# Kernel optimization log

Measured on AMD Instinct MI355X. Metric: run time of the kernel, lower is better.

The kernel has to match this reference:

```python
import jax, jax.numpy as jnp
import numpy as np

NUM_HEADS = 16


def setup_inputs() -> dict:
    key = jax.random.key(0)
    ks = jax.random.split(key, 5)
    N, L, E = 4, 1024, 1024
    x = jax.random.normal(ks[0], (N, L, E), dtype=jnp.float32)
    sc = 1.0 / np.sqrt(E)
    wq = jax.random.normal(ks[1], (E, E), dtype=jnp.float32) * sc
    wk = jax.random.normal(ks[2], (E, E), dtype=jnp.float32) * sc
    wv = jax.random.normal(ks[3], (E, E), dtype=jnp.float32) * sc
    wo = jax.random.normal(ks[4], (E, E), dtype=jnp.float32) * sc
    return {"x": x, "wq": wq, "wk": wk, "wv": wv, "wo": wo}


def reference(x, wq, wk, wv, wo):
    N, L, E = x.shape
    H = NUM_HEADS
    d = E // H  # d_k = d_v = d_q
    # Linear layers: y = x @ W^T (torch Linear weight is (out, in))
    q = (x @ wq.T).reshape(N, H, L, d)  # NOTE: raw view, matches torch .view
    k = (x @ wk.T).reshape(N, H, L, d)
    v = (x @ wv.T).reshape(N, H, L, d)
    scores = jnp.einsum("nhld,nhmd->nhlm", q, k) / jnp.sqrt(jnp.float32(d))
    # causal mask (dropout is identity in eval / p=0)
    causal = jnp.tril(jnp.ones((L, L), dtype=bool))
    scores = jnp.where(causal, scores, jnp.float32(-jnp.inf))
    attn = jax.nn.softmax(scores, axis=-1)
    wei = jnp.einsum("nhlm,nhmd->nhld", attn, v).reshape(N, L, H * d)
    return wei @ wo.T
```

## Files before the change

### kernel.cpp

```cpp
#include <hip/hip_runtime.h>
#include <hip/hip_bf16.h>

using bf16 = __hip_bfloat16;
typedef __attribute__((ext_vector_type(8))) short bf16x8;
typedef __attribute__((ext_vector_type(4))) float f32x4;

#define MFMA16(a, b, c) __builtin_amdgcn_mfma_f32_16x16x32_bf16(a, b, c, 0, 0, 0)
#define SWZ(row, byteoff) ((byteoff) ^ (((row) & 7) << 4))

__device__ __forceinline__ unsigned short f2b(float f) {
  union { float f; unsigned int u; } c; c.f = f;
  unsigned int r = c.u + 0x7fffu + ((c.u >> 16) & 1u);
  return (unsigned short)(r >> 16);
}
__device__ __forceinline__ float b2f(short b) {
  union { unsigned int u; float f; } c;
  c.u = ((unsigned int)(unsigned short)b) << 16;
  return c.f;
}
__device__ __forceinline__ bf16x8 scale8(bf16x8 v, float s) {
  bf16x8 r;
#pragma unroll
  for (int j = 0; j < 8; ++j) r[j] = (short)f2b(b2f(v[j]) * s);
  return r;
}
__device__ __forceinline__ unsigned cvtpk(float a, float b) {
  unsigned r;
  asm("v_cvt_pk_bf16_f32 %0, %1, %2" : "=v"(r) : "v"(a), "v"(b));
  return r;
}

__device__ __forceinline__ void gload_lds16(const void* g, void* l) {
  __builtin_amdgcn_global_load_lds(
      (const __attribute__((address_space(1))) void*)g,
      (__attribute__((address_space(3))) void*)l, 16, 0, 0);
}

__device__ __forceinline__ void store_out(float* p, float v) { *p = v; }
__device__ __forceinline__ void store_out(bf16* p, float v) {
  *(unsigned short*)p = f2b(v);
}

__global__ __launch_bounds__(256) void cast_all(
    const float* __restrict__ x, const float* __restrict__ wq,
    const float* __restrict__ wk, const float* __restrict__ wv,
    const float* __restrict__ wo,
    unsigned short* __restrict__ xb, unsigned short* __restrict__ wqb,
    unsigned short* __restrict__ wkb, unsigned short* __restrict__ wvb,
    unsigned short* __restrict__ wob) {
  int i = blockIdx.x * 256 + threadIdx.x;
  const float* src;
  unsigned short* dst;
  int off;
  if (i < 1048576) {
    src = x; dst = xb; off = i;
  } else {
    int j = i - 1048576;
    int seg = j >> 18;
    off = j & 262143;
    src = (seg == 0) ? wq : (seg == 1) ? wk : (seg == 2) ? wv : wo;
    dst = (seg == 0) ? wqb : (seg == 1) ? wkb : (seg == 2) ? wvb : wob;
  }
  float4 v = reinterpret_cast<const float4*>(src)[off];
  ushort4 o;
  o.x = f2b(v.x); o.y = f2b(v.y); o.z = f2b(v.z); o.w = f2b(v.w);
  reinterpret_cast<ushort4*>(dst)[off] = o;
}

template <typename TOUT>
__device__ __forceinline__ void gemm_tile(const bf16* __restrict__ A,
                                          const bf16* __restrict__ Bt,
                                          TOUT* __restrict__ C, int N, int K,
                                          int bm, int bn) {
  __shared__ bf16 Asm[128 * 64];
  __shared__ bf16 Bsm[128 * 64];
  const int tid = threadIdx.x;
  const int lane = tid & 63;
  const int w = tid >> 6;
  const int wr = w >> 1, wc = w & 1;
  const int fr = lane & 15;
  const int fg = lane >> 4;
  f32x4 acc[4][4] = {};

  const int strow = w * 8 + (lane >> 3);
  const int stcb = (lane & 7) * 16;

  for (int kt = 0; kt < K; kt += 64) {
#pragma unroll
    for (int r = 0; r < 4; ++r) {
      const int row = r * 32 + strow;
      gload_lds16(
          (const char*)(A + (size_t)(bm + row) * K + kt) + SWZ(row, stcb),
          (char*)Asm + (r * 32 + w * 8) * 128);
      gload_lds16(
          (const char*)(Bt + (size_t)row * K + kt) + SWZ(row, stcb),
          (char*)Bsm + (r * 32 + w * 8) * 128);
    }
    __syncthreads();
    bf16x8 afr[4][2], bfr[4][2];
#pragma unroll
    for (int m = 0; m < 4; ++m) {
      const int row = wr * 64 + m * 16 + fr;
      const char* rp = (const char*)Asm + row * 128;
#pragma unroll
      for (int s = 0; s < 2; ++s)
        afr[m][s] = *(const bf16x8*)(rp + SWZ(row, s * 64 + fg * 16));
    }
#pragma unroll
    for (int n = 0; n < 4; ++n) {
      const int row = wc * 64 + n * 16 + fr;
      const char* rp = (const char*)Bsm + row * 128;
#pragma unroll
      for (int s = 0; s < 2; ++s)
        bfr[n][s] = *(const bf16x8*)(rp + SWZ(row, s * 64 + fg * 16));
    }
    __builtin_amdgcn_s_setprio(1);
#pragma unroll
    for (int m = 0; m < 4; ++m)
#pragma unroll
      for (int n = 0; n < 4; ++n) {
        acc[m][n] = MFMA16(afr[m][0], bfr[n][0], acc[m][n]);
        acc[m][n] = MFMA16(afr[m][1], bfr[n][1], acc[m][n]);
      }
    __builtin_amdgcn_s_setprio(0);
    __syncthreads();
  }
#pragma unroll
  for (int m = 0; m < 4; ++m) {
    const int row0 = bm + wr * 64 + m * 16 + (lane >> 4) * 4;
#pragma unroll
    for (int n = 0; n < 4; ++n) {
      const int col = bn + wc * 64 + n * 16 + fr;
#pragma unroll
      for (int r = 0; r < 4; ++r)
        store_out(&C[(size_t)(row0 + r) * N + col], acc[m][n][r]);
    }
  }
}

__global__ __launch_bounds__(256) void gemm_qkv(
    const bf16* __restrict__ A, const bf16* __restrict__ B3,
    bf16* __restrict__ Cq, bf16* __restrict__ Ck, bf16* __restrict__ Cv) {
  const int id = blockIdx.y * 32 + blockIdx.x;
  const int sw = (id & 7) * 96 + (id >> 3);
  const int bm = (sw & 31) * 128;
  const int bnG = (sw >> 5) * 128;
  bf16* C = (bnG < 1024) ? Cq : (bnG < 2048) ? Ck : Cv;
  gemm_tile<bf16>(A, B3 + (size_t)bnG * 1024, C, 1024, 1024, bm, bnG & 1023);
}

__global__ __launch_bounds__(256) void gemm_out(const bf16* __restrict__ A,
                                                const bf16* __restrict__ B,
                                                float* __restrict__ C) {
  const int id = blockIdx.y * 32 + blockIdx.x;
  const int sw = (id & 7) * 32 + (id >> 3);
  const int bm = (sw & 31) * 128;
  const int bn = (sw >> 5) * 128;
  gemm_tile<float>(A, B + (size_t)bn * 1024, C, 1024, 1024, bm, bn);
}

__global__ __launch_bounds__(256) void attn_fwd(
    const bf16* __restrict__ Q, const bf16* __restrict__ K,
    const bf16* __restrict__ V, bf16* __restrict__ O) {
  const int nh = blockIdx.y;
  const size_t base = (size_t)nh * 65536;
  const bf16* Qp = Q + base;
  const bf16* Kp = K + base;
  const bf16* Vp = V + base;
  bf16* Op = O + base;
  const int p = blockIdx.x;
  const int qiA = p, qiB = 15 - p;
  const int tid = threadIdx.x;
  const int lane = tid & 63;
  const int w = tid >> 6;
  const int fr = lane & 15;
  const int fg = lane >> 4;

  __shared__ bf16 Ksm[2][64 * 64];
  __shared__ bf16 Vts[2][64 * 64];

  const float QSC = 0.125f * 1.44269504089f;
  const float MS = 12.0f;
  const int rA0 = qiA * 64 + w * 16;
  const int rB0 = qiB * 64 + w * 16;
  bf16x8 qA[2], qB[2];
#pragma unroll
  for (int ks = 0; ks < 2; ++ks) {
    qA[ks] = scale8(
        *(const bf16x8*)&Qp[(size_t)(rA0 + fr) * 64 + ks * 32 + fg * 8], QSC);
    qB[ks] = scale8(
        *(const bf16x8*)&Qp[(size_t)(rB0 + fr) * 64 + ks * 32 + fg * 8], QSC);
  }

  float sA = 0.f, sB = 0.f;
  f32x4 oA[4], oB[4];
#pragma unroll
  for (int d = 0; d < 4; ++d) {
    oA[d] = (f32x4){0.f, 0.f, 0.f, 0.f};
    oB[d] = (f32x4){0.f, 0.f, 0.f, 0.f};
  }

  const int NKV = qiB + 1;
  const int qloc = w * 16 + fr;

  const int bkv = (tid & 15) * 4;
  const int bd = (tid >> 4) * 4;
  union VU { ushort4 v; unsigned short s[4]; };
  VU v4[4], nv4[4];

  const int krow = w * 16 + (lane >> 3);
  const int kcb = (lane & 7) * 16;

#define STAGE_K(kt, bi)                                                       \
  {                                                                           \
    _Pragma("unroll") for (int i = 0; i < 2; ++i) {                           \
      const int row = krow + i * 8;                                           \
      gload_lds16((const char*)Kp + ((size_t)((kt)*64 + row) * 128 +          \
                                     SWZ(row, kcb)),                          \
                  (char*)&Ksm[bi][0] + (w * 16 + i * 8) * 128);               \
    }                                                                         \
  }
#define LOAD_V(kt, r)                                                         \
  {                                                                           \
    _Pragma("unroll") for (int j = 0; j < 4; ++j) (r)[j].v =                  \
        *(const ushort4*)(Vp + (size_t)((kt)*64 + bkv + j) * 64 + bd);        \
  }
#define WRITE_V(bi, r)                                                        \
  {                                                                           \
    _Pragma("unroll") for (int i = 0; i < 4; ++i) {                           \
      VU o4;                                                                  \
      _Pragma("unroll") for (int j = 0; j < 4; ++j) o4.s[j] = (r)[j].s[i];    \
      const int row = bd + i;                                                 \
      *(ushort4*)((char*)&Vts[bi][0] + row * 128 + SWZ(row, bkv * 2)) = o4.v; \
    }                                                                         \
  }

  STAGE_K(0, 0);
  LOAD_V(0, v4);
  WRITE_V(0, v4);
  __syncthreads();

  union PU { bf16x8 v; unsigned u[4]; };
  union VF { bf16x8 v; unsigned long long q[2]; };

  for (int kt = 0; kt < NKV; ++kt) {
    const int b = kt & 1;
    const bool more = (kt + 1 < NKV);
    if (more) {
      STAGE_K(kt + 1, b ^ 1);
      LOAD_V(kt + 1, nv4);
    }
    const bool aAct = (kt <= qiA);

    bf16x8 kf[4][2];
#pragma unroll
    for (int c = 0; c < 4; ++c) {
      const int row = c * 16 + fr;
      const char* rp = (const char*)&Ksm[b][0] + row * 128;
      kf[c][0] = *(const bf16x8*)(rp + SWZ(row, fg * 16));
      kf[c][1] = *(const bf16x8*)(rp + SWZ(row, 64 + fg * 16));
    }
    VF vf[4][2];
#pragma unroll
    for (int d = 0; d < 4; ++d) {
      const int row = d * 16 + fr;
      const char* rp = (const char*)&Vts[b][0] + row * 128;
#pragma unroll
      for (int ks = 0; ks < 2; ++ks) {
        vf[d][ks].q[0] =
            *(const unsigned long long*)(rp + SWZ(row, ks * 64 + fg * 8));
        vf[d][ks].q[1] =
            *(const unsigned long long*)(rp + SWZ(row, ks * 64 + 32 + fg * 8));
      }
    }

    auto strip_sm = [&](const bf16x8 (&qf)[2], float& s, bool diag,
                        PU (&pa)[2]) {
      f32x4 sc[4];
      __builtin_amdgcn_s_setprio(1);
#pragma unroll
      for (int c = 0; c < 4; ++c) {
        f32x4 acc = (f32x4){0.f, 0.f, 0.f, 0.f};
        acc = MFMA16(kf[c][0], qf[0], acc);
        acc = MFMA16(kf[c][1], qf[1], acc);
        sc[c] = acc;
      }
      __builtin_amdgcn_s_setprio(0);
      float pv[4][4];
#pragma unroll
      for (int c = 0; c < 4; ++c)
#pragma unroll
        for (int r = 0; r < 4; ++r) {
          float sv = sc[c][r];
          if (diag) {
            const int kvloc = c * 16 + fg * 4 + r;
            sv = (kvloc <= qloc) ? sv : -INFINITY;
          }
          const float e = __builtin_amdgcn_exp2f(sv - MS);
          pv[c][r] = e;
          s += e;
        }
#pragma unroll
      for (int ks = 0; ks < 2; ++ks) {
        pa[ks].u[0] = cvtpk(pv[ks * 2][0], pv[ks * 2][1]);
        pa[ks].u[1] = cvtpk(pv[ks * 2][2], pv[ks * 2][3]);
        pa[ks].u[2] = cvtpk(pv[ks * 2 + 1][0], pv[ks * 2 + 1][1]);
        pa[ks].u[3] = cvtpk(pv[ks * 2 + 1][2], pv[ks * 2 + 1][3]);
      }
    };

    PU paA[2], paB[2];
    strip_sm(qB, sB, kt == qiB, paB);
    if (aAct) strip_sm(qA, sA, kt == qiA, paA);

    __builtin_amdgcn_s_setprio(1);
#pragma unroll
    for (int d = 0; d < 4; ++d) {
      oB[d] = MFMA16(paB[0].v, vf[d][0].v, oB[d]);
      oB[d] = MFMA16(paB[1].v, vf[d][1].v, oB[d]);
    }
    if (aAct) {
#pragma unroll
      for (int d = 0; d < 4; ++d) {
        oA[d] = MFMA16(paA[0].v, vf[d][0].v, oA[d]);
        oA[d] = MFMA16(paA[1].v, vf[d][1].v, oA[d]);
      }
    }
    __builtin_amdgcn_s_setprio(0);

    if (more) WRITE_V(b ^ 1, nv4);
    __syncthreads();
  }

  sA += __shfl_xor(sA, 16); sA += __shfl_xor(sA, 32);
  sB += __shfl_xor(sB, 16); sB += __shfl_xor(sB, 32);
  float sAo[4], sBo[4];
#pragma unroll
  for (int r = 0; r < 4; ++r) {
    sAo[r] = __shfl(sA, fg * 4 + r);
    sBo[r] = __shfl(sB, fg * 4 + r);
  }

#pragma unroll
  for (int d = 0; d < 4; ++d)
#pragma unroll
    for (int r = 0; r < 4; ++r) {
      const float vA = oA[d][r] / sAo[r];
      const float vB = oB[d][r] / sBo[r];
      *(unsigned short*)&Op[(size_t)(rA0 + fg * 4 + r) * 64 + d * 16 + fr] =
          f2b(vA);
      *(unsigned short*)&Op[(size_t)(rB0 + fg * 4 + r) * 64 + d * 16 + fr] =
          f2b(vB);
    }
#undef STAGE_K
#undef LOAD_V
#undef WRITE_V
}

extern "C" void kernel_launch(void* const* d_in, const int* in_sizes, int n_in,
                              void* d_out, int out_size, void* d_ws,
                              size_t ws_size, hipStream_t stream) {
  const float* x = (const float*)d_in[0];
  const float* wq = (const float*)d_in[1];
  const float* wk = (const float*)d_in[2];
  const float* wv = (const float*)d_in[3];
  const float* wo = (const float*)d_in[4];
  float* out = (float*)d_out;
  char* ws = (char*)d_ws;

  bf16* xb = (bf16*)(ws);
  bf16* wqkv = (bf16*)(ws + (8u << 20));
  bf16* wqb = wqkv;
  bf16* wkb = (bf16*)(ws + (10u << 20));
  bf16* wvb = (bf16*)(ws + (12u << 20));
  bf16* wob = (bf16*)(ws + (14u << 20));
  bf16* qbuf = (bf16*)(ws + (16u << 20));
  bf16* kbuf = (bf16*)(ws + (24u << 20));
  bf16* vbuf = (bf16*)(ws + (32u << 20));
  bf16* weib = (bf16*)(ws);

  cast_all<<<8192, 256, 0, stream>>>(x, wq, wk, wv, wo, (unsigned short*)xb,
                                     (unsigned short*)wqb, (unsigned short*)wkb,
                                     (unsigned short*)wvb, (unsigned short*)wob);
  gemm_qkv<<<dim3(32, 24), 256, 0, stream>>>(xb, wqkv, qbuf, kbuf, vbuf);
  attn_fwd<<<dim3(8, 64), 256, 0, stream>>>(qbuf, kbuf, vbuf, weib);
  gemm_out<<<dim3(32, 8), 256, 0, stream>>>(weib, wob, out);
}
```

Measured before the change: 94.38 us.

## Split attention KV loop across two wave groups with LDS reduction

The attention kernel now launches 512 threads per block. Two halves of four waves each process alternating KV tiles, each half with its own double-buffered K/V region in a 64KB LDS array. At the end, the second half writes its partial output accumulators and row sums to LDS and the first half adds them before normalising and storing. The aim is to halve the serial KV-loop length per block and add more waves for latency hiding. The cost is more LDS use, an extra reduction step, and the V prefetch now being written synchronously rather than kept in registers across compute.

```diff
diff --git a/kernel.cpp b/kernel.cpp
--- a/kernel.cpp
+++ b/kernel.cpp
@@ -159,7 +159,7 @@
   gemm_tile<float>(A, B + (size_t)bn * 1024, C, 1024, 1024, bm, bn);
 }
 
-__global__ __launch_bounds__(256) void attn_fwd(
+__global__ __launch_bounds__(512, 4) void attn_fwd(
     const bf16* __restrict__ Q, const bf16* __restrict__ K,
     const bf16* __restrict__ V, bf16* __restrict__ O) {
   const int nh = blockIdx.y;
@@ -172,17 +172,20 @@
   const int qiA = p, qiB = 15 - p;
   const int tid = threadIdx.x;
   const int lane = tid & 63;
-  const int w = tid >> 6;
+  const int w8 = tid >> 6;
+  const int half = w8 >> 2;
+  const int wv = w8 & 3;
+  const int tid_h = tid & 255;
   const int fr = lane & 15;
   const int fg = lane >> 4;
 
-  __shared__ bf16 Ksm[2][64 * 64];
-  __shared__ bf16 Vts[2][64 * 64];
+  __shared__ __align__(16) char ldsraw[65536];
+  float* Xch = (float*)ldsraw;
 
   const float QSC = 0.125f * 1.44269504089f;
   const float MS = 12.0f;
-  const int rA0 = qiA * 64 + w * 16;
-  const int rB0 = qiB * 64 + w * 16;
+  const int rA0 = qiA * 64 + wv * 16;
+  const int rB0 = qiB * 64 + wv * 16;
   bf16x8 qA[2], qB[2];
 #pragma unroll
   for (int ks = 0; ks < 2; ++ks) {
@@ -201,157 +204,189 @@
   }
 
   const int NKV = qiB + 1;
-  const int qloc = w * 16 + fr;
-
-  const int bkv = (tid & 15) * 4;
-  const int bd = (tid >> 4) * 4;
+  const int qloc = wv * 16 + fr;
+
+  const int bkv = (tid_h & 15) * 4;
+  const int bd = (tid_h >> 4) * 4;
   union VU { ushort4 v; unsigned short s[4]; };
-  VU v4[4], nv4[4];
-
-  const int krow = w * 16 + (lane >> 3);
+  VU v4[4];
+
+  const int krow = wv * 16 + (lane >> 3);
   const int kcb = (lane & 7) * 16;
 
-#define STAGE_K(kt, bi)                                                       \
-  {                                                                           \
-    _Pragma("unroll") for (int i = 0; i < 2; ++i) {                           \
-      const int row = krow + i * 8;                                           \
-      gload_lds16((const char*)Kp + ((size_t)((kt)*64 + row) * 128 +          \
-                                     SWZ(row, kcb)),                          \
-                  (char*)&Ksm[bi][0] + (w * 16 + i * 8) * 128);               \
-    }                                                                         \
-  }
-#define LOAD_V(kt, r)                                                         \
-  {                                                                           \
-    _Pragma("unroll") for (int j = 0; j < 4; ++j) (r)[j].v =                  \
-        *(const ushort4*)(Vp + (size_t)((kt)*64 + bkv + j) * 64 + bd);        \
-  }
-#define WRITE_V(bi, r)                                                        \
-  {                                                                           \
-    _Pragma("unroll") for (int i = 0; i < 4; ++i) {                           \
-      VU o4;                                                                  \
-      _Pragma("unroll") for (int j = 0; j < 4; ++j) o4.s[j] = (r)[j].s[i];    \
-      const int row = bd + i;                                                 \
-      *(ushort4*)((char*)&Vts[bi][0] + row * 128 + SWZ(row, bkv * 2)) = o4.v; \
-    }                                                                         \
-  }
-
-  STAGE_K(0, 0);
-  LOAD_V(0, v4);
+#define KBASE(bi) (ldsraw + half * 16384 + (bi)*8192)
+#define VBASE(bi) (ldsraw + 32768 + half * 16384 + (bi)*8192)
+#define STAGE_K(kt, bi)                                                     \
+  {                                                                         \
+    _Pragma("unroll") for (int i = 0; i < 2; ++i) {                         \
+      const int row = krow + i * 8;                                         \
+      gload_lds16((const char*)Kp + ((size_t)((kt)*64 + row) * 128 +        \
+                                     SWZ(row, kcb)),                        \
+                  KBASE(bi) + (wv * 16 + i * 8) * 128);                     \
+    }                                                                       \
+  }
+#define LOAD_V(kt, r)                                                       \
+  {                                                                         \
+    _Pragma("unroll") for (int j = 0; j < 4; ++j) (r)[j].v =                \
+        *(const ushort4*)(Vp + (size_t)((kt)*64 + bkv + j) * 64 + bd);      \
+  }
+#define WRITE_V(bi, r)                                                      \
+  {                                                                         \
+    _Pragma("unroll") for (int i = 0; i < 4; ++i) {                         \
+      VU o4;                                                                \
+      _Pragma("unroll") for (int j = 0; j < 4; ++j) o4.s[j] = (r)[j].s[i];  \
+      const int row = bd + i;                                               \
+      *(ushort4*)(VBASE(bi) + row * 128 + SWZ(row, bkv * 2)) = o4.v;        \
+    }                                                                       \
+  }
+
+  STAGE_K(half, 0);
+  LOAD_V(half, v4);
   WRITE_V(0, v4);
   __syncthreads();
 
   union PU { bf16x8 v; unsigned u[4]; };
   union VF { bf16x8 v; unsigned long long q[2]; };
 
-  for (int kt = 0; kt < NKV; ++kt) {
-    const int b = kt & 1;
-    const bool more = (kt + 1 < NKV);
-    if (more) {
-      STAGE_K(kt + 1, b ^ 1);
-      LOAD_V(kt + 1, nv4);
-    }
-    const bool aAct = (kt <= qiA);
-
-    bf16x8 kf[4][2];
-#pragma unroll
-    for (int c = 0; c < 4; ++c) {
-      const int row = c * 16 + fr;
-      const char* rp = (const char*)&Ksm[b][0] + row * 128;
-      kf[c][0] = *(const bf16x8*)(rp + SWZ(row, fg * 16));
-      kf[c][1] = *(const bf16x8*)(rp + SWZ(row, 64 + fg * 16));
-    }
-    VF vf[4][2];
-#pragma unroll
-    for (int d = 0; d < 4; ++d) {
-      const int row = d * 16 + fr;
-      const char* rp = (const char*)&Vts[b][0] + row * 128;
-#pragma unroll
-      for (int ks = 0; ks < 2; ++ks) {
-        vf[d][ks].q[0] =
-            *(const unsigned long long*)(rp + SWZ(row, ks * 64 + fg * 8));
-        vf[d][ks].q[1] =
-            *(const unsigned long long*)(rp + SWZ(row, ks * 64 + 32 + fg * 8));
-      }
-    }
-
-    auto strip_sm = [&](const bf16x8 (&qf)[2], float& s, bool diag,
-                        PU (&pa)[2]) {
-      f32x4 sc[4];
+  const int I = (NKV + 1) >> 1;
+  for (int i = 0; i < I; ++i) {
+    const int kt = 2 * i + half;
+    const int b = i & 1;
+    const bool act = kt < NKV;
+    const int ktn = kt + 2;
+    if (ktn < NKV) {
+      STAGE_K(ktn, b ^ 1);
+      LOAD_V(ktn, v4);
+      WRITE_V(b ^ 1, v4);
+    }
+
+    if (act) {
+      const bool aAct = (kt <= qiA);
+      bf16x8 kf[4][2];
+#pragma unroll
+      for (int c = 0; c < 4; ++c) {
+        const int row = c * 16 + fr;
+        const char* rp = KBASE(b) + row * 128;
+        kf[c][0] = *(const bf16x8*)(rp + SWZ(row, fg * 16));
+        kf[c][1] = *(const bf16x8*)(rp + SWZ(row, 64 + fg * 16));
+      }
+      VF vf[4][2];
+#pragma unroll
+      for (int d = 0; d < 4; ++d) {
+        const int row = d * 16 + fr;
+        const char* rp = VBASE(b) + row * 128;
+#pragma unroll
+        for (int ks = 0; ks < 2; ++ks) {
+          vf[d][ks].q[0] =
+              *(const unsigned long long*)(rp + SWZ(row, ks * 64 + fg * 8));
+          vf[d][ks].q[1] = *(const unsigned long long*)(rp +
+                               SWZ(row, ks * 64 + 32 + fg * 8));
+        }
+      }
+
+      auto strip_sm = [&](const bf16x8 (&qf)[2], float& s, bool diag,
+                          PU (&pa)[2]) {
+        f32x4 sc[4];
+        __builtin_amdgcn_s_setprio(1);
+#pragma unroll
+        for (int c = 0; c < 4; ++c) {
+          f32x4 acc = (f32x4){0.f, 0.f, 0.f, 0.f};
+          acc = MFMA16(kf[c][0], qf[0], acc);
+          acc = MFMA16(kf[c][1], qf[1], acc);
+          sc[c] = acc;
+        }
+        __builtin_amdgcn_s_setprio(0);
+        float pv[4][4];
+#pragma unroll
+        for (int c = 0; c < 4; ++c)
+#pragma unroll
+          for (int r = 0; r < 4; ++r) {
+            float sv = sc[c][r];
+            if (diag) {
+              const int kvloc = c * 16 + fg * 4 + r;
+              sv = (kvloc <= qloc) ? sv : -INFINITY;
+            }
+            const float e = __builtin_amdgcn_exp2f(sv - MS);
+            pv[c][r] = e;
+            s += e;
+          }
+#pragma unroll
+        for (int ks = 0; ks < 2; ++ks) {
+          pa[ks].u[0] = cvtpk(pv[ks * 2][0], pv[ks * 2][1]);
+          pa[ks].u[1] = cvtpk(pv[ks * 2][2], pv[ks * 2][3]);
+          pa[ks].u[2] = cvtpk(pv[ks * 2 + 1][0], pv[ks * 2 + 1][1]);
+          pa[ks].u[3] = cvtpk(pv[ks * 2 + 1][2], pv[ks * 2 + 1][3]);
+        }
+      };
+
+      PU paA[2], paB[2];
+      strip_sm(qB, sB, kt == qiB, paB);
+      if (aAct) strip_sm(qA, sA, kt == qiA, paA);
+
       __builtin_amdgcn_s_setprio(1);
 #pragma unroll
-      for (int c = 0; c < 4; ++c) {
-        f32x4 acc = (f32x4){0.f, 0.f, 0.f, 0.f};
-        acc = MFMA16(kf[c][0], qf[0], acc);
-        acc = MFMA16(kf[c][1], qf[1], acc);
-        sc[c] = acc;
+      for (int d = 0; d < 4; ++d) {
+        oB[d] = MFMA16(paB[0].v, vf[d][0].v, oB[d]);
+        oB[d] = MFMA16(paB[1].v, vf[d][1].v, oB[d]);
+      }
+      if (aAct) {
+#pragma unroll
+        for (int d = 0; d < 4; ++d) {
+          oA[d] = MFMA16(paA[0].v, vf[d][0].v, oA[d]);
+          oA[d] = MFMA16(paA[1].v, vf[d][1].v, oA[d]);
+        }
       }
       __builtin_amdgcn_s_setprio(0);
-      float pv[4][4];
-#pragma unroll
-      for (int c = 0; c < 4; ++c)
-#pragma unroll
-        for (int r = 0; r < 4; ++r) {
-          float sv = sc[c][r];
-          if (diag) {
-            const int kvloc = c * 16 + fg * 4 + r;
-            sv = (kvloc <= qloc) ? sv : -INFINITY;
-          }
-          const float e = __builtin_amdgcn_exp2f(sv - MS);
-          pv[c][r] = e;
-          s += e;
-        }
-#pragma unroll
-      for (int ks = 0; ks < 2; ++ks) {
-        pa[ks].u[0] = cvtpk(pv[ks * 2][0], pv[ks * 2][1]);
-        pa[ks].u[1] = cvtpk(pv[ks * 2][2], pv[ks * 2][3]);
-        pa[ks].u[2] = cvtpk(pv[ks * 2 + 1][0], pv[ks * 2 + 1][1]);
-        pa[ks].u[3] = cvtpk(pv[ks * 2 + 1][2], pv[ks * 2 + 1][3]);
-      }
-    };
-
-    PU paA[2], paB[2];
-    strip_sm(qB, sB, kt == qiB, paB);
-    if (aAct) strip_sm(qA, sA, kt == qiA, paA);
-
-    __builtin_amdgcn_s_setprio(1);
-#pragma unroll
-    for (int d = 0; d < 4; ++d) {
-      oB[d] = MFMA16(paB[0].v, vf[d][0].v, oB[d]);
-      oB[d] = MFMA16(paB[1].v, vf[d][1].v, oB[d]);
-    }
-    if (aAct) {
-#pragma unroll
-      for (int d = 0; d < 4; ++d) {
-        oA[d] = MFMA16(paA[0].v, vf[d][0].v, oA[d]);
-        oA[d] = MFMA16(paA[1].v, vf[d][1].v, oA[d]);
-      }
-    }
-    __builtin_amdgcn_s_setprio(0);
-
-    if (more) WRITE_V(b ^ 1, nv4);
+    }
     __syncthreads();
   }
 
   sA += __shfl_xor(sA, 16); sA += __shfl_xor(sA, 32);
   sB += __shfl_xor(sB, 16); sB += __shfl_xor(sB, 32);
-  float sAo[4], sBo[4];
-#pragma unroll
-  for (int r = 0; r < 4; ++r) {
-    sAo[r] = __shfl(sA, fg * 4 + r);
-    sBo[r] = __shfl(sB, fg * 4 + r);
-  }
-
-#pragma unroll
-  for (int d = 0; d < 4; ++d)
+
+  float* X = &Xch[(wv * 64 + lane) * 34];
+  if (half == 1) {
+#pragma unroll
+    for (int d = 0; d < 4; ++d)
+#pragma unroll
+      for (int r = 0; r < 4; ++r) {
+        X[d * 4 + r] = oA[d][r];
+        X[16 + d * 4 + r] = oB[d][r];
+      }
+    X[32] = sA;
+    X[33] = sB;
+  }
+  __syncthreads();
+  if (half == 0) {
+#pragma unroll
+    for (int d = 0; d < 4; ++d)
+#pragma unroll
+      for (int r = 0; r < 4; ++r) {
+        oA[d][r] += X[d * 4 + r];
+        oB[d][r] += X[16 + d * 4 + r];
+      }
+    sA += X[32];
+    sB += X[33];
+    float sAo[4], sBo[4];
 #pragma unroll
     for (int r = 0; r < 4; ++r) {
-      const float vA = oA[d][r] / sAo[r];
-      const float vB = oB[d][r] / sBo[r];
-      *(unsigned short*)&Op[(size_t)(rA0 + fg * 4 + r) * 64 + d * 16 + fr] =
-          f2b(vA);
-      *(unsigned short*)&Op[(size_t)(rB0 + fg * 4 + r) * 64 + d * 16 + fr] =
-          f2b(vB);
-    }
+      sAo[r] = __shfl(sA, fg * 4 + r);
+      sBo[r] = __shfl(sB, fg * 4 + r);
+    }
+#pragma unroll
+    for (int d = 0; d < 4; ++d)
+#pragma unroll
+      for (int r = 0; r < 4; ++r) {
+        const float vA = oA[d][r] / sAo[r];
+        const float vB = oB[d][r] / sBo[r];
+        *(unsigned short*)&Op[(size_t)(rA0 + fg * 4 + r) * 64 + d * 16 + fr] =
+            f2b(vA);
+        *(unsigned short*)&Op[(size_t)(rB0 + fg * 4 + r) * 64 + d * 16 + fr] =
+            f2b(vB);
+      }
+  }
+#undef KBASE
+#undef VBASE
 #undef STAGE_K
 #undef LOAD_V
 #undef WRITE_V
@@ -383,6 +418,6 @@
                                      (unsigned short*)wqb, (unsigned short*)wkb,
                                      (unsigned short*)wvb, (unsigned short*)wob);
   gemm_qkv<<<dim3(32, 24), 256, 0, stream>>>(xb, wqkv, qbuf, kbuf, vbuf);
-  attn_fwd<<<dim3(8, 64), 256, 0, stream>>>(qbuf, kbuf, vbuf, weib);
+  attn_fwd<<<dim3(8, 64), 512, 0, stream>>>(qbuf, kbuf, vbuf, weib);
   gemm_out<<<dim3(32, 8), 256, 0, stream>>>(weib, wob, out);
 }
```

Result: slower. 151.5 us (+60.5%).
